# Kernel optimization log

Hardware: AMD Instinct MI355X
Metric: run time of the kernel (lower is better)

The kernel has to match this reference:

```python
import jax, jax.numpy as jnp
import numpy as np
import math

D_MODEL = 1024
NUM_HEADS = 16  # scale = sqrt(D_MODEL / NUM_HEADS)
BATCH, SEQ = 4, 4096


def setup_inputs() -> dict:
    key = jax.random.key(0)
    ks = jax.random.split(key, 7)
    s = 1.0 / math.sqrt(D_MODEL)
    return {
        "query": jax.random.normal(ks[0], (BATCH, SEQ, D_MODEL), jnp.float32),
        "value": jax.random.normal(ks[1], (BATCH, SEQ, D_MODEL), jnp.float32),
        "Wq": jax.random.normal(ks[2], (D_MODEL, D_MODEL), jnp.float32) * s,
        "bq": jax.random.normal(ks[3], (D_MODEL,), jnp.float32) * s,
        "qk_b": jnp.zeros((D_MODEL,), jnp.float32),
        "Wv": jax.random.normal(ks[4], (D_MODEL, D_MODEL), jnp.float32) * s,
        "bv": jax.random.normal(ks[5], (D_MODEL,), jnp.float32) * s,
    }


def reference(query, value, Wq, bq, qk_b, Wv, bv):
    # q_proj = Linear(query) + extra bias qk_b ; v_proj = Linear(value)
    q = jnp.einsum("bsd,ed->bse", query, Wq) + bq + qk_b   # [B,S,D]
    v = jnp.einsum("bsd,ed->bse", value, Wv) + bv          # [B,S,D]
    inv_scale = math.sqrt(query.shape[-1] / NUM_HEADS)
    scores = jnp.einsum("bqd,bkd->bqk", q, v) / inv_scale  # [B,S,S]
    attn = jax.nn.softmax(scores, axis=-1)
    # dropout_p = 0.0 -> identity
    return jnp.einsum("bqk,bkd->bqd", attn, v)             # [B,S,D]
```

## Files before the change

kernel.cpp:

```cpp
#include <hip/hip_runtime.h>

#define B_ 4
#define S_ 4096
#define D_ 1024

typedef __bf16 bf16;
typedef _Float16 f16;
typedef __attribute__((ext_vector_type(8))) __bf16 bf16x8;
typedef __attribute__((ext_vector_type(8))) _Float16 f16x8;
typedef __attribute__((ext_vector_type(4))) float floatx4;

__device__ inline floatx4 mfma16(bf16x8 a, bf16x8 b, floatx4 c) {
    return __builtin_amdgcn_mfma_f32_16x16x32_bf16(a, b, c, 0, 0, 0);
}
__device__ inline floatx4 mfma_any(bf16x8 a, bf16x8 b, floatx4 c) {
    return __builtin_amdgcn_mfma_f32_16x16x32_bf16(a, b, c, 0, 0, 0);
}
__device__ inline floatx4 mfma_any(f16x8 a, f16x8 b, floatx4 c) {
    return __builtin_amdgcn_mfma_f32_16x16x32_f16(a, b, c, 0, 0, 0);
}

template <typename T> struct vec8_of;
template <> struct vec8_of<bf16> { using type = bf16x8; };
template <> struct vec8_of<f16>  { using type = f16x8; };

__device__ inline bf16x8 cvt8(float4 a, float4 b) {
    bf16x8 h;
    h[0] = (bf16)a.x; h[1] = (bf16)a.y; h[2] = (bf16)a.z; h[3] = (bf16)a.w;
    h[4] = (bf16)b.x; h[5] = (bf16)b.y; h[6] = (bf16)b.z; h[7] = (bf16)b.w;
    return h;
}

__global__ __launch_bounds__(256) void cast_f32_bf16(
    const float* __restrict__ in, bf16* __restrict__ out)
{
    size_t i = ((size_t)blockIdx.x * 256 + threadIdx.x) * 8;
    float4 a = *(const float4*)(in + i);
    float4 b = *(const float4*)(in + i + 4);
    *(bf16x8*)(out + i) = cvt8(a, b);
}

template <typename TI, typename TO, bool HAS_BIAS>
__global__ __launch_bounds__(256) void gemm128(
    const TI* __restrict__ A, const TI* __restrict__ B, TO* __restrict__ C,
    int K, int ldc, size_t strideA, size_t strideB, size_t strideC,
    const float* __restrict__ bias1, const float* __restrict__ bias2, float scale)
{
    using v8 = typename vec8_of<TI>::type;
    __shared__ TI sA[2 * 128 * 32];
    __shared__ TI sB[2 * 128 * 32];
    A += (size_t)blockIdx.z * strideA;
    B += (size_t)blockIdx.z * strideB;
    C += (size_t)blockIdx.z * strideC;

    const int tid = threadIdx.x;
    const int wave = tid >> 6, lane = tid & 63, quad = lane >> 4, l16 = lane & 15;
    const int m0 = blockIdx.x * 128, n0 = blockIdx.y * 128;
    const int wr = (wave >> 1) * 64, wc = (wave & 1) * 64;

    floatx4 acc[4][4];
#pragma unroll
    for (int i = 0; i < 4; i++)
#pragma unroll
        for (int j = 0; j < 4; j++) acc[i][j] = (floatx4)0.0f;

    for (int k0 = 0; k0 < K; k0 += 64) {
#pragma unroll
        for (int s = 0; s < 2; s++) {
#pragma unroll
            for (int j = 0; j < 2; j++) {
                int idx = j * 256 + tid;
                int r = idx >> 2, c = (idx & 3) * 8;
                __builtin_amdgcn_global_load_lds(
                    (const __attribute__((address_space(1))) void*)(A + (size_t)(m0 + r) * K + k0 + s * 32 + c),
                    (__attribute__((address_space(3))) void*)(sA + s * 4096 + idx * 8), 16, 0, 0);
                __builtin_amdgcn_global_load_lds(
                    (const __attribute__((address_space(1))) void*)(B + (size_t)(n0 + r) * K + k0 + s * 32 + c),
                    (__attribute__((address_space(3))) void*)(sB + s * 4096 + idx * 8), 16, 0, 0);
            }
        }
        __syncthreads();
#pragma unroll
        for (int s = 0; s < 2; s++) {
            v8 af[4], bfv[4];
#pragma unroll
            for (int i = 0; i < 4; i++) {
                af[i]  = *(const v8*)&sA[s * 4096 + (wr + i * 16 + l16) * 32 + quad * 8];
                bfv[i] = *(const v8*)&sB[s * 4096 + (wc + i * 16 + l16) * 32 + quad * 8];
            }
#pragma unroll
            for (int mf = 0; mf < 4; mf++)
#pragma unroll
                for (int nf = 0; nf < 4; nf++)
                    acc[mf][nf] = mfma_any(af[mf], bfv[nf], acc[mf][nf]);
        }
        __syncthreads();
    }

#pragma unroll
    for (int mf = 0; mf < 4; mf++)
#pragma unroll
        for (int nf = 0; nf < 4; nf++) {
            int col = n0 + wc + nf * 16 + l16;
            float badd = 0.0f;
            if (HAS_BIAS) {
                badd = bias1[col];
                if (bias2) badd += bias2[col];
            }
#pragma unroll
            for (int r = 0; r < 4; r++) {
                int row = m0 + wr + mf * 16 + quad * 4 + r;
                float v = acc[mf][nf][r];
                if (HAS_BIAS) v = (v + badd) * scale;
                C[(size_t)row * ldc + col] = (TO)v;
            }
        }
}

__global__ __launch_bounds__(256) void transpose_v(
    const bf16* __restrict__ vb, bf16* __restrict__ vtb)
{
    __shared__ bf16 tile[32][33];
    const int b = blockIdx.z;
    const int s0 = blockIdx.x * 32, d0 = blockIdx.y * 32;
    const int tr = threadIdx.x >> 5;
    const int tc = threadIdx.x & 31;
#pragma unroll
    for (int k = 0; k < 4; k++) {
        int r = tr + k * 8;
        tile[r][tc] = vb[((size_t)b * S_ + s0 + r) * D_ + d0 + tc];
    }
    __syncthreads();
#pragma unroll
    for (int k = 0; k < 4; k++) {
        int r = tr + k * 8;
        vtb[((size_t)b * D_ + d0 + r) * S_ + s0 + tc] = tile[tc][r];
    }
}

__global__ __launch_bounds__(256) void transpose_v_f16(
    const bf16* __restrict__ vb, f16* __restrict__ vtb)
{
    __shared__ bf16 tile[32][33];
    const int b = blockIdx.z;
    const int s0 = blockIdx.x * 32, d0 = blockIdx.y * 32;
    const int tr = threadIdx.x >> 5;
    const int tc = threadIdx.x & 31;
#pragma unroll
    for (int k = 0; k < 4; k++) {
        int r = tr + k * 8;
        tile[r][tc] = vb[((size_t)b * S_ + s0 + r) * D_ + d0 + tc];
    }
    __syncthreads();
#pragma unroll
    for (int k = 0; k < 4; k++) {
        int r = tr + k * 8;
        vtb[((size_t)b * D_ + d0 + r) * S_ + s0 + tc] = (f16)(float)tile[tc][r];
    }
}

__global__ __launch_bounds__(256) void softmax_inplace_f16(f16* __restrict__ Sc)
{
    f16* row = Sc + (size_t)blockIdx.x * S_;
    const int tid = threadIdx.x, wave = tid >> 6, lane = tid & 63;
    __shared__ float redm[4], redl[4];

    f16x8 a = *(const f16x8*)(row + tid * 16);
    f16x8 b = *(const f16x8*)(row + tid * 16 + 8);
    float v[16];
#pragma unroll
    for (int j = 0; j < 8; j++) { v[j] = (float)a[j]; v[8 + j] = (float)b[j]; }

    float m = -1e30f;
#pragma unroll
    for (int j = 0; j < 16; j++) m = fmaxf(m, v[j]);
#pragma unroll
    for (int off = 32; off; off >>= 1) m = fmaxf(m, __shfl_xor(m, off));
    if (lane == 0) redm[wave] = m;
    __syncthreads();
    m = fmaxf(fmaxf(redm[0], redm[1]), fmaxf(redm[2], redm[3]));

    float s = 0.0f;
#pragma unroll
    for (int j = 0; j < 16; j++) { v[j] = __expf(v[j] - m); s += v[j]; }
#pragma unroll
    for (int off = 32; off; off >>= 1) s += __shfl_xor(s, off);
    if (lane == 0) redl[wave] = s;
    __syncthreads();
    s = redl[0] + redl[1] + redl[2] + redl[3];
    float inv = 1.0f / s;

#pragma unroll
    for (int j = 0; j < 8; j++) { a[j] = (f16)(v[j] * inv); b[j] = (f16)(v[8 + j] * inv); }
    *(f16x8*)(row + tid * 16) = a;
    *(f16x8*)(row + tid * 16 + 8) = b;
}

__global__ __launch_bounds__(256) void softmax_row(
    const float* __restrict__ Sc, f16* __restrict__ P)
{
    const int q = blockIdx.x;
    const float* row = Sc + (size_t)q * S_;
    f16* prow = P + (size_t)q * S_;
    const int tid = threadIdx.x, wave = tid >> 6, lane = tid & 63;

    float4 v[4];
#pragma unroll
    for (int i = 0; i < 4; i++) v[i] = *(const float4*)(row + tid * 16 + i * 4);

    float m = -1e30f;
#pragma unroll
    for (int i = 0; i < 4; i++)
        m = fmaxf(m, fmaxf(fmaxf(v[i].x, v[i].y), fmaxf(v[i].z, v[i].w)));
#pragma unroll
    for (int off = 32; off; off >>= 1) m = fmaxf(m, __shfl_xor(m, off));
    __shared__ float redm[4], redl[4];
    if (lane == 0) redm[wave] = m;
    __syncthreads();
    m = fmaxf(fmaxf(redm[0], redm[1]), fmaxf(redm[2], redm[3]));

    float p[16];
    float s = 0.0f;
#pragma unroll
    for (int i = 0; i < 4; i++) {
        p[i * 4 + 0] = __expf(v[i].x - m);
        p[i * 4 + 1] = __expf(v[i].y - m);
        p[i * 4 + 2] = __expf(v[i].z - m);
        p[i * 4 + 3] = __expf(v[i].w - m);
        s += p[i * 4] + p[i * 4 + 1] + p[i * 4 + 2] + p[i * 4 + 3];
    }
#pragma unroll
    for (int off = 32; off; off >>= 1) s += __shfl_xor(s, off);
    if (lane == 0) redl[wave] = s;
    __syncthreads();
    s = redl[0] + redl[1] + redl[2] + redl[3];
    float inv = 1.0f / s;

    f16x8 o0, o1;
#pragma unroll
    for (int j = 0; j < 8; j++) {
        o0[j] = (f16)(p[j] * inv);
        o1[j] = (f16)(p[8 + j] * inv);
    }
    *(f16x8*)(prow + tid * 16) = o0;
    *(f16x8*)(prow + tid * 16 + 8) = o1;
}

#define SSTR 40
__global__ __launch_bounds__(256) void proj_gemm(
    const float* __restrict__ A, const float* __restrict__ W,
    const float* __restrict__ bias1, const float* __restrict__ bias2,
    bf16* __restrict__ C, float scale)
{
    __shared__ bf16 sA[64 * SSTR];
    __shared__ bf16 sB[64 * SSTR];
    const int tid = threadIdx.x;
    const int wave = tid >> 6, lane = tid & 63, quad = lane >> 4, l16 = lane & 15;
    const int m0 = blockIdx.x * 64, n0 = blockIdx.y * 64;
    const int wr = (wave >> 1) * 32, wc = (wave & 1) * 32;
    const int lr = tid >> 2;
    const int lc = (tid & 3) * 8;

    floatx4 acc[2][2];
#pragma unroll
    for (int i = 0; i < 2; i++)
#pragma unroll
        for (int j = 0; j < 2; j++) acc[i][j] = (floatx4)0.0f;

    for (int k0 = 0; k0 < 1024; k0 += 32) {
        const float* ga = A + (size_t)(m0 + lr) * 1024 + k0 + lc;
        const float* gw = W + (size_t)(n0 + lr) * 1024 + k0 + lc;
        float4 a0 = *(const float4*)ga;
        float4 a1 = *(const float4*)(ga + 4);
        float4 w0 = *(const float4*)gw;
        float4 w1 = *(const float4*)(gw + 4);
        *(bf16x8*)&sA[lr * SSTR + lc] = cvt8(a0, a1);
        *(bf16x8*)&sB[lr * SSTR + lc] = cvt8(w0, w1);
        __syncthreads();
        bf16x8 af[2], bfv[2];
        af[0]  = *(bf16x8*)&sA[(wr + l16) * SSTR + quad * 8];
        af[1]  = *(bf16x8*)&sA[(wr + 16 + l16) * SSTR + quad * 8];
        bfv[0] = *(bf16x8*)&sB[(wc + l16) * SSTR + quad * 8];
        bfv[1] = *(bf16x8*)&sB[(wc + 16 + l16) * SSTR + quad * 8];
#pragma unroll
        for (int mf = 0; mf < 2; mf++)
#pragma unroll
            for (int nf = 0; nf < 2; nf++)
                acc[mf][nf] = mfma16(af[mf], bfv[nf], acc[mf][nf]);
        __syncthreads();
    }
#pragma unroll
    for (int mf = 0; mf < 2; mf++)
#pragma unroll
        for (int nf = 0; nf < 2; nf++) {
            int col = n0 + wc + nf * 16 + l16;
            float bsum = bias1[col] + (bias2 ? bias2[col] : 0.0f);
#pragma unroll
            for (int r = 0; r < 4; r++) {
                int row = m0 + wr + mf * 16 + quad * 4 + r;
                C[(size_t)row * 1024 + col] = (bf16)((acc[mf][nf][r] + bsum) * scale);
            }
        }
}

#define BR 32
#define TK 64
#define DC 256
__global__ __launch_bounds__(256, 2) void flash_attn(
    const bf16* __restrict__ qb, const bf16* __restrict__ vb,
    const bf16* __restrict__ vtb, float* __restrict__ out)
{
    __shared__ float sPart[4][32][65];
    __shared__ bf16 sP[32][72];
    __shared__ float sM[32], sL[32], sAlpha[32];

    const int tid = threadIdx.x;
    const int wave = tid >> 6, lane = tid & 63, quad = lane >> 4, l16 = lane & 15;
    const int b = blockIdx.y, q0 = blockIdx.x * BR;

    bf16x8 qf[2][8];
#pragma unroll
    for (int mf = 0; mf < 2; mf++)
#pragma unroll
        for (int ks = 0; ks < 8; ks++) {
            int row = q0 + mf * 16 + l16;
            int col = wave * DC + ks * 32 + quad * 8;
            qf[mf][ks] = *(const bf16x8*)(qb + ((size_t)b * S_ + row) * D_ + col);
        }

    floatx4 o[2][16];
#pragma unroll
    for (int mf = 0; mf < 2; mf++)
#pragma unroll
        for (int nf = 0; nf < 16; nf++) o[mf][nf] = (floatx4)0.0f;

    if (tid < 32) { sM[tid] = -1e30f; sL[tid] = 0.0f; }
    __syncthreads();

    for (int kt = 0; kt < S_ / TK; kt++) {
        const int k0 = kt * TK;
        floatx4 sp[2][4];
#pragma unroll
        for (int mf = 0; mf < 2; mf++)
#pragma unroll
            for (int nf = 0; nf < 4; nf++) sp[mf][nf] = (floatx4)0.0f;
#pragma unroll
        for (int ks = 0; ks < 8; ks++) {
            int col = wave * DC + ks * 32 + quad * 8;
#pragma unroll
            for (int nf = 0; nf < 4; nf++) {
                int key = k0 + nf * 16 + l16;
                bf16x8 vf = *(const bf16x8*)(vb + ((size_t)b * S_ + key) * D_ + col);
                sp[0][nf] = mfma16(qf[0][ks], vf, sp[0][nf]);
                sp[1][nf] = mfma16(qf[1][ks], vf, sp[1][nf]);
            }
        }
#pragma unroll
        for (int mf = 0; mf < 2; mf++)
#pragma unroll
            for (int nf = 0; nf < 4; nf++)
#pragma unroll
                for (int r = 0; r < 4; r++)
                    sPart[wave][mf * 16 + quad * 4 + r][nf * 16 + l16] = sp[mf][nf][r];
        __syncthreads();

        {
            const int rr = tid >> 3, c0 = (tid & 7) * 8;
            float v[8];
            float mx = -1e30f;
#pragma unroll
            for (int j = 0; j < 8; j++) {
                v[j] = sPart[0][rr][c0 + j] + sPart[1][rr][c0 + j] +
                       sPart[2][rr][c0 + j] + sPart[3][rr][c0 + j];
                mx = fmaxf(mx, v[j]);
            }
            mx = fmaxf(mx, __shfl_xor(mx, 1));
            mx = fmaxf(mx, __shfl_xor(mx, 2));
            mx = fmaxf(mx, __shfl_xor(mx, 4));
            float m_old = sM[rr];
            float m_new = fmaxf(m_old, mx);
            float rsum = 0.0f;
#pragma unroll
            for (int j = 0; j < 8; j++) {
                float p = __expf(v[j] - m_new);
                sP[rr][c0 + j] = (bf16)p;
                rsum += p;
            }
            rsum += __shfl_xor(rsum, 1);
            rsum += __shfl_xor(rsum, 2);
            rsum += __shfl_xor(rsum, 4);
            if ((tid & 7) == 0) {
                float alpha = __expf(m_old - m_new);
                sAlpha[rr] = alpha;
                sM[rr] = m_new;
                sL[rr] = sL[rr] * alpha + rsum;
            }
        }
        __syncthreads();

        float al[2][4];
#pragma unroll
        for (int mf = 0; mf < 2; mf++)
#pragma unroll
            for (int r = 0; r < 4; r++) al[mf][r] = sAlpha[mf * 16 + quad * 4 + r];
#pragma unroll
        for (int mf = 0; mf < 2; mf++)
#pragma unroll
            for (int nf = 0; nf < 16; nf++)
#pragma unroll
                for (int r = 0; r < 4; r++) o[mf][nf][r] *= al[mf][r];

#pragma unroll
        for (int ks2 = 0; ks2 < 2; ks2++) {
            bf16x8 pA[2];
            pA[0] = *(bf16x8*)&sP[l16][ks2 * 32 + quad * 8];
            pA[1] = *(bf16x8*)&sP[16 + l16][ks2 * 32 + quad * 8];
            int key = k0 + ks2 * 32 + quad * 8;
#pragma unroll
            for (int nf = 0; nf < 16; nf++) {
                int d = wave * DC + nf * 16 + l16;
                bf16x8 vtf = *(const bf16x8*)(vtb + ((size_t)b * D_ + d) * S_ + key);
                o[0][nf] = mfma16(pA[0], vtf, o[0][nf]);
                o[1][nf] = mfma16(pA[1], vtf, o[1][nf]);
            }
        }
        __syncthreads();
    }

#pragma unroll
    for (int mf = 0; mf < 2; mf++) {
        float inv[4];
#pragma unroll
        for (int r = 0; r < 4; r++) inv[r] = 1.0f / sL[mf * 16 + quad * 4 + r];
#pragma unroll
        for (int nf = 0; nf < 16; nf++) {
            int d = wave * DC + nf * 16 + l16;
#pragma unroll
            for (int r = 0; r < 4; r++) {
                int row = q0 + mf * 16 + quad * 4 + r;
                out[((size_t)b * S_ + row) * D_ + d] = o[mf][nf][r] * inv[r];
            }
        }
    }
}

extern "C" void kernel_launch(void* const* d_in, const int* in_sizes, int n_in,
                              void* d_out, int out_size, void* d_ws, size_t ws_size,
                              hipStream_t stream) {
    const float* query = (const float*)d_in[0];
    const float* value = (const float*)d_in[1];
    const float* Wq    = (const float*)d_in[2];
    const float* bq    = (const float*)d_in[3];
    const float* qk_b  = (const float*)d_in[4];
    const float* Wv    = (const float*)d_in[5];
    const float* bv    = (const float*)d_in[6];
    float* out = (float*)d_out;

    const size_t SD = (size_t)S_ * D_;
    const size_t SS = (size_t)S_ * S_;
    const size_t MB = 1024 * 1024;

    char* w = (char*)d_ws;
    bf16* qb = (bf16*)w;
    bf16* vb = (bf16*)(w + 32 * MB);

    if (ws_size >= 224 * MB) {
        f16* vtb = (f16*)(w + 64 * MB);
        f16* Sc  = (f16*)(w + 96 * MB);
        bf16* qc  = (bf16*)(w + 96 * MB);
        bf16* vc  = (bf16*)(w + 128 * MB);
        bf16* wqc = (bf16*)(w + 160 * MB);
        bf16* wvc = (bf16*)(w + 163 * MB);

        cast_f32_bf16<<<(B_ * SD) / 2048, 256, 0, stream>>>(query, qc);
        cast_f32_bf16<<<(B_ * SD) / 2048, 256, 0, stream>>>(value, vc);
        cast_f32_bf16<<<((size_t)D_ * D_) / 2048, 256, 0, stream>>>(Wq, wqc);
        cast_f32_bf16<<<((size_t)D_ * D_) / 2048, 256, 0, stream>>>(Wv, wvc);

        gemm128<bf16, bf16, true><<<dim3(128, 8, 1), 256, 0, stream>>>(
            qc, wqc, qb, D_, D_, 0, 0, 0, bq, qk_b, 0.125f);
        gemm128<bf16, bf16, true><<<dim3(128, 8, 1), 256, 0, stream>>>(
            vc, wvc, vb, D_, D_, 0, 0, 0, bv, nullptr, 1.0f);

        transpose_v_f16<<<dim3(S_ / 32, D_ / 32, B_), 256, 0, stream>>>(vb, vtb);

        gemm128<bf16, f16, false><<<dim3(32, 32, B_), 256, 0, stream>>>(
            qb, vb, Sc, D_, S_, SD, SD, SS, nullptr, nullptr, 1.0f);

        softmax_inplace_f16<<<B_ * S_, 256, 0, stream>>>(Sc);

        gemm128<f16, float, false><<<dim3(32, 8, B_), 256, 0, stream>>>(
            Sc, vtb, out, S_, D_, SS, (size_t)D_ * S_, SD, nullptr, nullptr, 1.0f);
    } else if (ws_size >= 192 * MB) {
        f16*   vtb = (f16*)(w + 64 * MB);
        float* Sc  = (float*)(w + 96 * MB);
        f16*   Pn  = (f16*)(w + 160 * MB);
        bf16*  qc  = (bf16*)(w + 96 * MB);
        bf16*  vc  = (bf16*)(w + 128 * MB);
        bf16*  wqc = (bf16*)(w + 160 * MB);
        bf16*  wvc = (bf16*)(w + 163 * MB);

        cast_f32_bf16<<<(B_ * SD) / 2048, 256, 0, stream>>>(query, qc);
        cast_f32_bf16<<<(B_ * SD) / 2048, 256, 0, stream>>>(value, vc);
        cast_f32_bf16<<<((size_t)D_ * D_) / 2048, 256, 0, stream>>>(Wq, wqc);
        cast_f32_bf16<<<((size_t)D_ * D_) / 2048, 256, 0, stream>>>(Wv, wvc);

        gemm128<bf16, bf16, true><<<dim3(128, 8, 1), 256, 0, stream>>>(
            qc, wqc, qb, D_, D_, 0, 0, 0, bq, qk_b, 0.125f);
        gemm128<bf16, bf16, true><<<dim3(128, 8, 1), 256, 0, stream>>>(
            vc, wvc, vb, D_, D_, 0, 0, 0, bv, nullptr, 1.0f);

        transpose_v_f16<<<dim3(S_ / 32, D_ / 32, B_), 256, 0, stream>>>(vb, vtb);

        for (int b = 0; b < B_; b++) {
            gemm128<bf16, float, false><<<dim3(32, 32, 1), 256, 0, stream>>>(
                qb + b * SD, vb + b * SD, Sc, D_, S_, 0, 0, 0, nullptr, nullptr, 1.0f);
            softmax_row<<<S_, 256, 0, stream>>>(Sc, Pn);
            gemm128<f16, float, false><<<dim3(32, 8, 1), 256, 0, stream>>>(
                Pn, vtb + (size_t)b * D_ * S_, out + b * SD, S_, D_,
                0, 0, 0, nullptr, nullptr, 1.0f);
        }
    } else {
        bf16* vtb = (bf16*)(w + 64 * MB);
        dim3 pg(16384 / 64, 1024 / 64);
        proj_gemm<<<pg, 256, 0, stream>>>(query, Wq, bq, qk_b, qb, 0.125f);
        proj_gemm<<<pg, 256, 0, stream>>>(value, Wv, bv, nullptr, vb, 1.0f);
        transpose_v<<<dim3(S_ / 32, D_ / 32, B_), 256, 0, stream>>>(vb, vtb);
        flash_attn<<<dim3(S_ / BR, B_), 256, 0, stream>>>(qb, vb, vtb, out);
    }
}
```

Measured before the change: 673.7 us.

## Add 256x256-tile 8-wave GEMM with direct-to-LDS loads and swizzled grid

Adds a new GEMM kernel with 256x256 output tiles, 512 threads and a K step of 64. Operands are staged into XOR-swizzled LDS with global_load_lds, and the A and B halves are pipelined against MFMA phases using barriers and s_setprio. Block indices are remapped so tiles that share inputs run together, and all four GEMMs in the main path switch to this kernel. The larger tiles raise data reuse and cut global traffic. The cost is heavier register and LDS use per block, and the last PV GEMM runs only 256 blocks, which could leave some CUs idle.

```diff
diff --git a/kernel.cpp b/kernel.cpp
--- a/kernel.cpp
+++ b/kernel.cpp
@@ -38,6 +38,178 @@
     float4 a = *(const float4*)(in + i);
     float4 b = *(const float4*)(in + i + 4);
     *(bf16x8*)(out + i) = cvt8(a, b);
+}
+
+template <typename TI, typename TO, bool HAS_BIAS>
+__global__ __launch_bounds__(512, 2) void gemm256(
+    const TI* __restrict__ A, const TI* __restrict__ B, TO* __restrict__ C,
+    int K, int ldc, size_t strideA, size_t strideB, size_t strideC,
+    const float* __restrict__ bias1, const float* __restrict__ bias2,
+    float scale, int tiles_n)
+{
+    using v8 = typename vec8_of<TI>::type;
+    __shared__ __align__(16) TI sA[2][2][8192];
+    __shared__ __align__(16) TI sB[2][2][8192];
+
+    A += (size_t)blockIdx.z * strideA;
+    B += (size_t)blockIdx.z * strideB;
+    C += (size_t)blockIdx.z * strideC;
+
+    const int tid = threadIdx.x;
+    const int wave = tid >> 6, lane = tid & 63, quad = lane >> 4, l16 = lane & 15;
+    const int wm = wave >> 2, wn = wave & 3;
+
+    const int gx = gridDim.x;
+    const int cpx = gx >> 3;
+    const int lid = (blockIdx.x & 7) * cpx + (blockIdx.x >> 3);
+    const int tm = lid / tiles_n, tn = lid - tm * tiles_n;
+    const int m0 = tm * 256, n0 = tn * 256;
+
+    int r_[2], c_[2];
+#pragma unroll
+    for (int j = 0; j < 2; j++) {
+        int idx = j * 512 + tid;
+        int dB = idx * 16;
+        int L = dB ^ (((dB >> 7) & 7) << 4);
+        r_[j] = L >> 7;
+        c_[j] = (L & 127) >> 1;
+    }
+    const int NT = K >> 6;
+
+    auto stageA = [&](int t, int half, int bufsel) {
+#pragma unroll
+        for (int j = 0; j < 2; j++) {
+            int idx = j * 512 + tid;
+            __builtin_amdgcn_global_load_lds(
+                (const __attribute__((address_space(1))) void*)(
+                    A + (size_t)(m0 + half * 128 + r_[j]) * K + t * 64 + c_[j]),
+                (__attribute__((address_space(3))) void*)(sA[bufsel][half] + idx * 8),
+                16, 0, 0);
+        }
+    };
+    auto stageB = [&](int t, int half, int bufsel) {
+#pragma unroll
+        for (int j = 0; j < 2; j++) {
+            int idx = j * 512 + tid;
+            __builtin_amdgcn_global_load_lds(
+                (const __attribute__((address_space(1))) void*)(
+                    B + (size_t)(n0 + half * 128 + r_[j]) * K + t * 64 + c_[j]),
+                (__attribute__((address_space(3))) void*)(sB[bufsel][half] + idx * 8),
+                16, 0, 0);
+        }
+    };
+    auto rdA = [&](int buf, int i, int q) -> v8 {
+        int row = i * 16 + l16;
+        int byte = (row * 128 + q * 64 + quad * 16) ^ ((row & 7) << 4);
+        return *(const v8*)((const char*)(sA[buf][wm]) + byte);
+    };
+    auto rdB = [&](int buf, int j, int q) -> v8 {
+        int row = (wn & 1) * 64 + j * 16 + l16;
+        int byte = (row * 128 + q * 64 + quad * 16) ^ ((row & 7) << 4);
+        return *(const v8*)((const char*)(sB[buf][wn >> 1]) + byte);
+    };
+
+    floatx4 acc[8][4];
+#pragma unroll
+    for (int i = 0; i < 8; i++)
+#pragma unroll
+        for (int j = 0; j < 4; j++) acc[i][j] = (floatx4)0.0f;
+
+    {
+        int t1 = (1 < NT) ? 1 : NT - 1;
+        stageA(0, 0, 0); stageA(0, 1, 0);
+        stageB(0, 0, 0); stageB(0, 1, 0);
+        stageB(t1, 0, 1); stageB(t1, 1, 1);
+        asm volatile("s_waitcnt vmcnt(4)" ::: "memory");
+        __builtin_amdgcn_s_barrier();
+    }
+
+    v8 a[8], b0[4], b1[4];
+    for (int t = 0; t < NT; t++) {
+        const int buf = t & 1;
+        const int tA = (t + 1 < NT) ? t + 1 : NT - 1;
+        const int tB = (t + 2 < NT) ? t + 2 : NT - 1;
+
+#pragma unroll
+        for (int i = 0; i < 4; i++) { a[2 * i] = rdA(buf, i, 0); a[2 * i + 1] = rdA(buf, i, 1); }
+#pragma unroll
+        for (int j = 0; j < 2; j++) { b0[2 * j] = rdB(buf, j, 0); b0[2 * j + 1] = rdB(buf, j, 1); }
+        stageA(tA, 0, buf ^ 1);
+        __builtin_amdgcn_s_barrier();
+        __builtin_amdgcn_s_setprio(1);
+#pragma unroll
+        for (int i = 0; i < 4; i++)
+#pragma unroll
+            for (int j = 0; j < 2; j++) {
+                acc[i][j] = mfma_any(a[2 * i], b0[2 * j], acc[i][j]);
+                acc[i][j] = mfma_any(a[2 * i + 1], b0[2 * j + 1], acc[i][j]);
+            }
+        __builtin_amdgcn_s_setprio(0);
+        __builtin_amdgcn_s_barrier();
+
+#pragma unroll
+        for (int j = 0; j < 2; j++) { b1[2 * j] = rdB(buf, 2 + j, 0); b1[2 * j + 1] = rdB(buf, 2 + j, 1); }
+        stageA(tA, 1, buf ^ 1);
+        __builtin_amdgcn_s_barrier();
+        __builtin_amdgcn_s_setprio(1);
+#pragma unroll
+        for (int i = 0; i < 4; i++)
+#pragma unroll
+            for (int j = 0; j < 2; j++) {
+                acc[i][2 + j] = mfma_any(a[2 * i], b1[2 * j], acc[i][2 + j]);
+                acc[i][2 + j] = mfma_any(a[2 * i + 1], b1[2 * j + 1], acc[i][2 + j]);
+            }
+        __builtin_amdgcn_s_setprio(0);
+        __builtin_amdgcn_s_barrier();
+
+#pragma unroll
+        for (int i = 0; i < 4; i++) { a[2 * i] = rdA(buf, 4 + i, 0); a[2 * i + 1] = rdA(buf, 4 + i, 1); }
+        stageB(tB, 0, buf);
+        __builtin_amdgcn_s_barrier();
+        __builtin_amdgcn_s_setprio(1);
+#pragma unroll
+        for (int i = 0; i < 4; i++)
+#pragma unroll
+            for (int j = 0; j < 2; j++) {
+                acc[4 + i][2 + j] = mfma_any(a[2 * i], b1[2 * j], acc[4 + i][2 + j]);
+                acc[4 + i][2 + j] = mfma_any(a[2 * i + 1], b1[2 * j + 1], acc[4 + i][2 + j]);
+            }
+        __builtin_amdgcn_s_setprio(0);
+        __builtin_amdgcn_s_barrier();
+
+        stageB(tB, 1, buf);
+        asm volatile("s_waitcnt vmcnt(4)" ::: "memory");
+        __builtin_amdgcn_s_barrier();
+        __builtin_amdgcn_s_setprio(1);
+#pragma unroll
+        for (int i = 0; i < 4; i++)
+#pragma unroll
+            for (int j = 0; j < 2; j++) {
+                acc[4 + i][j] = mfma_any(a[2 * i], b0[2 * j], acc[4 + i][j]);
+                acc[4 + i][j] = mfma_any(a[2 * i + 1], b0[2 * j + 1], acc[4 + i][j]);
+            }
+        __builtin_amdgcn_s_setprio(0);
+        __builtin_amdgcn_s_barrier();
+    }
+
+#pragma unroll
+    for (int mf = 0; mf < 8; mf++)
+#pragma unroll
+        for (int nf = 0; nf < 4; nf++) {
+            int col = n0 + wn * 64 + nf * 16 + l16;
+            float badd = 0.0f;
+            if (HAS_BIAS) {
+                badd = bias1[col];
+                if (bias2) badd += bias2[col];
+            }
+#pragma unroll
+            for (int r = 0; r < 4; r++) {
+                int row = m0 + wm * 128 + mf * 16 + quad * 4 + r;
+                float v = acc[mf][nf][r];
+                if (HAS_BIAS) v = (v + badd) * scale;
+                C[(size_t)row * ldc + col] = (TO)v;
+            }
+        }
 }
 
 template <typename TI, typename TO, bool HAS_BIAS>
@@ -477,20 +649,20 @@
         cast_f32_bf16<<<((size_t)D_ * D_) / 2048, 256, 0, stream>>>(Wq, wqc);
         cast_f32_bf16<<<((size_t)D_ * D_) / 2048, 256, 0, stream>>>(Wv, wvc);
 
-        gemm128<bf16, bf16, true><<<dim3(128, 8, 1), 256, 0, stream>>>(
-            qc, wqc, qb, D_, D_, 0, 0, 0, bq, qk_b, 0.125f);
-        gemm128<bf16, bf16, true><<<dim3(128, 8, 1), 256, 0, stream>>>(
-            vc, wvc, vb, D_, D_, 0, 0, 0, bv, nullptr, 1.0f);
+        gemm256<bf16, bf16, true><<<dim3(256, 1, 1), 512, 0, stream>>>(
+            qc, wqc, qb, D_, D_, 0, 0, 0, bq, qk_b, 0.125f, 4);
+        gemm256<bf16, bf16, true><<<dim3(256, 1, 1), 512, 0, stream>>>(
+            vc, wvc, vb, D_, D_, 0, 0, 0, bv, nullptr, 1.0f, 4);
 
         transpose_v_f16<<<dim3(S_ / 32, D_ / 32, B_), 256, 0, stream>>>(vb, vtb);
 
-        gemm128<bf16, f16, false><<<dim3(32, 32, B_), 256, 0, stream>>>(
-            qb, vb, Sc, D_, S_, SD, SD, SS, nullptr, nullptr, 1.0f);
+        gemm256<bf16, f16, false><<<dim3(256, 1, B_), 512, 0, stream>>>(
+            qb, vb, Sc, D_, S_, SD, SD, SS, nullptr, nullptr, 1.0f, 16);
 
         softmax_inplace_f16<<<B_ * S_, 256, 0, stream>>>(Sc);
 
-        gemm128<f16, float, false><<<dim3(32, 8, B_), 256, 0, stream>>>(
-            Sc, vtb, out, S_, D_, SS, (size_t)D_ * S_, SD, nullptr, nullptr, 1.0f);
+        gemm256<f16, float, false><<<dim3(64, 1, B_), 512, 0, stream>>>(
+            Sc, vtb, out, S_, D_, SS, (size_t)D_ * S_, SD, nullptr, nullptr, 1.0f, 4);
     } else if (ws_size >= 192 * MB) {
         f16*   vtb = (f16*)(w + 64 * MB);
         float* Sc  = (float*)(w + 96 * MB);
```

Result: faster. 587.2 us (-12.8%).
